# Kernel optimization log

Hardware: AMD Instinct MI355X
Metric: run time of the kernel (lower is better)

## Reference

```python
import jax, jax.numpy as jnp
import numpy as np

SIZE = 4096
DOWN = SIZE // 16  # reduction_factor = 16 -> 256
N_TASKS = 16
BATCH = 2048
INIT_STD = 0.01


def setup_inputs() -> dict:
    key = jax.random.key(0)
    k_x, k_t, k_wd, k_wu = jax.random.split(key, 4)
    x = jax.random.normal(k_x, (BATCH, SIZE), dtype=jnp.float32)
    task_id = jax.random.randint(k_t, (BATCH,), 0, N_TASKS)
    # Stacked per-task adapter params (init: normal(std=0.01) weights, zero bias)
    Wd = jax.random.normal(k_wd, (N_TASKS, SIZE, DOWN), dtype=jnp.float32) * INIT_STD
    bd = jnp.zeros((N_TASKS, DOWN), dtype=jnp.float32)
    Wu = jax.random.normal(k_wu, (N_TASKS, DOWN, SIZE), dtype=jnp.float32) * INIT_STD
    bu = jnp.zeros((N_TASKS, SIZE), dtype=jnp.float32)
    return {"x": x, "task_id": task_id, "Wd": Wd, "bd": bd, "Wu": Wu, "bu": bu}


def reference(x, task_id, Wd, bd, Wu, bu):
    # Down-projection for all tasks, then select each sample's routed task.
    # [B, T, DOWN] is small (B*T*256), cheaper than gathering [B, SIZE, DOWN] weights.
    down_all = jnp.einsum('bd,tdh->bth', x, Wd) + bd[None]
    down = jnp.take_along_axis(down_all, task_id[:, None, None], axis=1)[:, 0]  # [B, DOWN]
    act = jax.nn.silu(down)
    # Up-projection for all tasks, select routed task. [B, T, SIZE]
    up_all = jnp.einsum('bh,thd->btd', act, Wu) + bu[None]
    up = jnp.take_along_axis(up_all, task_id[:, None, None], axis=1)[:, 0]  # [B, SIZE]
    return x + up  # residual=True (default)
```

## Files before the change

### kernel.cpp

```cpp
#include <hip/hip_runtime.h>

#define BATCH 2048
#define SIZE 4096
#define DOWN 256
#define NTASK 16
#define KC 16
#define KCHUNK (SIZE / KC)

typedef _Float16 half8 __attribute__((ext_vector_type(8)));
typedef _Float16 half4 __attribute__((ext_vector_type(4)));
typedef float floatx4 __attribute__((ext_vector_type(4)));

__device__ __forceinline__ int imin(int a, int b) { return a < b ? a : b; }

__global__ __launch_bounds__(256) void sort_kernel(const int* __restrict__ task_id,
                                                   int* __restrict__ taskOff,
                                                   int* __restrict__ sortedIdx,
                                                   int* __restrict__ taskOfPos) {
    __shared__ int cnt[NTASK];
    __shared__ int base[NTASK + 1];
    __shared__ int cur[NTASK];
    int tid = threadIdx.x;
    if (tid < NTASK) cnt[tid] = 0;
    __syncthreads();
    for (int i = tid; i < BATCH; i += 256) atomicAdd(&cnt[task_id[i]], 1);
    __syncthreads();
    if (tid == 0) {
        int s = 0;
        for (int t = 0; t < NTASK; t++) { base[t] = s; s += cnt[t]; }
        base[NTASK] = s;
    }
    __syncthreads();
    if (tid < NTASK) { cur[tid] = base[tid]; taskOff[tid] = base[tid]; }
    if (tid == 0) taskOff[NTASK] = BATCH;
    __syncthreads();
    for (int i = tid; i < BATCH; i += 256) {
        int t = task_id[i];
        int p = atomicAdd(&cur[t], 1);
        sortedIdx[p] = i;
        taskOfPos[p] = t;
    }
}

__global__ __launch_bounds__(256, 2) void gemm1_kernel(const float* __restrict__ x,
                                                       const float* __restrict__ Wd,
                                                       const int* __restrict__ taskOff,
                                                       const int* __restrict__ sortedIdx,
                                                       _Float16* __restrict__ partial) {
    int task = blockIdx.x >> 1, z = blockIdx.x & 1, kc = blockIdx.y;
    int rowStart = taskOff[task];
    int nrows = taskOff[task + 1] - rowStart;
    if (nrows <= 0) return;

    __shared__ half8 A_lds[32][64];
    __shared__ half8 B_lds[4][64][8];

    int tid = threadIdx.x;
    int wave = tid >> 6, lane = tid & 63, quad = lane >> 4, l15 = lane & 15;
    int kbase = kc * KCHUNK;
    const float* Wdt = Wd + (size_t)task * SIZE * DOWN;
    int arow = tid >> 2, ac = tid & 3;

    for (int r0 = z * 64; r0 < nrows; r0 += 128) {
        __syncthreads();
        {
            int asrc = sortedIdx[rowStart + imin(r0 + arow, nrows - 1)];
            const float* xr = x + (size_t)asrc * SIZE + kbase;
            floatx4 f[16];
#pragma unroll
            for (int i = 0; i < 16; i++)
                f[i] = *(const floatx4*)(xr + i * 16 + ac * 4);
#pragma unroll
            for (int i = 0; i < 16; i++) {
                half4 h;
                h[0] = (_Float16)f[i][0]; h[1] = (_Float16)f[i][1];
                h[2] = (_Float16)f[i][2]; h[3] = (_Float16)f[i][3];
                int kg = i * 2 + (ac >> 1);
                *((half4*)(&A_lds[kg][arow]) + (ac & 1)) = h;
            }
        }
        __syncthreads();

        floatx4 acc[4][4];
#pragma unroll
        for (int mi = 0; mi < 4; mi++)
#pragma unroll
            for (int ni = 0; ni < 4; ni++) acc[mi][ni] = (floatx4){0.f, 0.f, 0.f, 0.f};

        for (int kb = 0; kb < KCHUNK; kb += 64) {
            floatx4 fb[16];
            const float* bs =
                Wdt + (size_t)(kbase + kb + quad * 16) * DOWN + wave * 64 + l15 * 4;
#pragma unroll
            for (int j = 0; j < 16; j++) fb[j] = *(const floatx4*)(bs + (size_t)j * DOWN);
#pragma unroll
            for (int g = 0; g < 2; g++)
#pragma unroll
                for (int n2 = 0; n2 < 4; n2++) {
                    half8 h;
#pragma unroll
                    for (int e = 0; e < 8; e++) h[e] = (_Float16)fb[g * 8 + e][n2];
                    B_lds[wave][l15 * 4 + n2][quad * 2 + g] = h;
                }
#pragma unroll
            for (int ks = 0; ks < 2; ks++) {
                int kg = (kb >> 3) + ks * 4 + quad;
                half8 a[4], b[4];
#pragma unroll
                for (int i = 0; i < 4; i++) a[i] = A_lds[kg][i * 16 + l15];
#pragma unroll
                for (int i = 0; i < 4; i++) b[i] = B_lds[wave][i * 16 + l15][ks * 4 + quad];
#pragma unroll
                for (int mi = 0; mi < 4; mi++)
#pragma unroll
                    for (int ni = 0; ni < 4; ni++)
                        acc[mi][ni] = __builtin_amdgcn_mfma_f32_16x16x32_f16(
                            a[mi], b[ni], acc[mi][ni], 0, 0, 0);
            }
        }
#pragma unroll
        for (int mi = 0; mi < 4; mi++) {
#pragma unroll
            for (int reg = 0; reg < 4; reg++) {
                int r = r0 + mi * 16 + quad * 4 + reg;
                if (r < nrows) {
                    size_t rowoff = ((size_t)kc * BATCH + (rowStart + r)) * DOWN;
#pragma unroll
                    for (int ni = 0; ni < 4; ni++) {
                        int h = wave * 64 + ni * 16 + l15;
                        partial[rowoff + h] = (_Float16)acc[mi][ni][reg];
                    }
                }
            }
        }
    }
}

__global__ __launch_bounds__(256) void silu_kernel(const _Float16* __restrict__ partial,
                                                   const float* __restrict__ bd,
                                                   const int* __restrict__ taskOfPos,
                                                   _Float16* __restrict__ act) {
    int idx = blockIdx.x * 256 + threadIdx.x;
    int s = idx >> 5;
    int h = (idx & 31) * 8;
    int t = taskOfPos[s];
    floatx4 b0 = *(const floatx4*)(bd + t * DOWN + h);
    floatx4 b1 = *(const floatx4*)(bd + t * DOWN + h + 4);
    float v[8];
    v[0] = b0[0]; v[1] = b0[1]; v[2] = b0[2]; v[3] = b0[3];
    v[4] = b1[0]; v[5] = b1[1]; v[6] = b1[2]; v[7] = b1[3];
#pragma unroll
    for (int kc = 0; kc < KC; kc++) {
        half8 p = *(const half8*)(partial + ((size_t)kc * BATCH + s) * DOWN + h);
#pragma unroll
        for (int j = 0; j < 8; j++) v[j] += (float)p[j];
    }
    half8 o;
#pragma unroll
    for (int j = 0; j < 8; j++) {
        float sv = v[j] / (1.0f + __expf(-v[j]));
        o[j] = (_Float16)sv;
    }
    *(half8*)(act + (size_t)s * DOWN + h) = o;
}

__global__ __launch_bounds__(256, 2) void gemm2_kernel(const _Float16* __restrict__ act,
                                                       const float* __restrict__ Wu,
                                                       const float* __restrict__ bu,
                                                       const float* __restrict__ x,
                                                       const int* __restrict__ taskOff,
                                                       const int* __restrict__ sortedIdx,
                                                       float* __restrict__ out) {
    int nt = blockIdx.x >> 1, z = blockIdx.x & 1, task = blockIdx.y;
    int rowStart = taskOff[task];
    int nrows = taskOff[task + 1] - rowStart;
    if (nrows <= 0) return;

    __shared__ half8 A_lds[32][64];
    __shared__ half8 B_lds[4][64][8];

    int tid = threadIdx.x;
    int wave = tid >> 6, lane = tid & 63, quad = lane >> 4, l15 = lane & 15;
    int ncol0 = nt * 256;
    const float* Wut = Wu + (size_t)task * DOWN * SIZE;
    int arow = tid >> 2, ac = tid & 3;

    for (int r0 = z * 64; r0 < nrows; r0 += 128) {
        __syncthreads();
        {
            int s_a = rowStart + imin(r0 + arow, nrows - 1);
            const _Float16* ar = act + (size_t)s_a * DOWN;
#pragma unroll
            for (int j = 0; j < 8; j++) {
                int kg = j * 4 + ac;
                A_lds[kg][arow] = *(const half8*)(ar + kg * 8);
            }
        }
        __syncthreads();

        floatx4 acc[4][4];
#pragma unroll
        for (int mi = 0; mi < 4; mi++)
#pragma unroll
            for (int ni = 0; ni < 4; ni++) acc[mi][ni] = (floatx4){0.f, 0.f, 0.f, 0.f};

        for (int kb = 0; kb < DOWN; kb += 64) {
            floatx4 fb[16];
            const float* bs =
                Wut + (size_t)(kb + quad * 16) * SIZE + ncol0 + wave * 64 + l15 * 4;
#pragma unroll
            for (int j = 0; j < 16; j++) fb[j] = *(const floatx4*)(bs + (size_t)j * SIZE);
#pragma unroll
            for (int g = 0; g < 2; g++)
#pragma unroll
                for (int n2 = 0; n2 < 4; n2++) {
                    half8 h;
#pragma unroll
                    for (int e = 0; e < 8; e++) h[e] = (_Float16)fb[g * 8 + e][n2];
                    B_lds[wave][l15 * 4 + n2][quad * 2 + g] = h;
                }
#pragma unroll
            for (int ks = 0; ks < 2; ks++) {
                int kg = (kb >> 3) + ks * 4 + quad;
                half8 a[4], b[4];
#pragma unroll
                for (int i = 0; i < 4; i++) a[i] = A_lds[kg][i * 16 + l15];
#pragma unroll
                for (int i = 0; i < 4; i++) b[i] = B_lds[wave][i * 16 + l15][ks * 4 + quad];
#pragma unroll
                for (int mi = 0; mi < 4; mi++)
#pragma unroll
                    for (int ni = 0; ni < 4; ni++)
                        acc[mi][ni] = __builtin_amdgcn_mfma_f32_16x16x32_f16(
                            a[mi], b[ni], acc[mi][ni], 0, 0, 0);
            }
        }
#pragma unroll
        for (int mi = 0; mi < 4; mi++) {
#pragma unroll
            for (int reg = 0; reg < 4; reg++) {
                int r = r0 + mi * 16 + quad * 4 + reg;
                if (r < nrows) {
                    int b = sortedIdx[rowStart + r];
                    const float* xr = x + (size_t)b * SIZE;
                    float* outr = out + (size_t)b * SIZE;
#pragma unroll
                    for (int ni = 0; ni < 4; ni++) {
                        int n = ncol0 + wave * 64 + ni * 16 + l15;
                        outr[n] = acc[mi][ni][reg] + bu[task * SIZE + n] + xr[n];
                    }
                }
            }
        }
    }
}

extern "C" void kernel_launch(void* const* d_in, const int* in_sizes, int n_in,
                              void* d_out, int out_size, void* d_ws, size_t ws_size,
                              hipStream_t stream) {
    const float* x       = (const float*)d_in[0];
    const int*   task_id = (const int*)d_in[1];
    const float* Wd      = (const float*)d_in[2];
    const float* bd      = (const float*)d_in[3];
    const float* Wu      = (const float*)d_in[4];
    const float* bu      = (const float*)d_in[5];
    float* out = (float*)d_out;

    _Float16* partial = (_Float16*)d_out;
    _Float16* act     = (_Float16*)d_ws;
    int* taskOff   = (int*)(act + (size_t)BATCH * DOWN);
    int* sortedIdx = taskOff + 32;
    int* taskOfPos = sortedIdx + BATCH;

    sort_kernel<<<1, 256, 0, stream>>>(task_id, taskOff, sortedIdx, taskOfPos);
    gemm1_kernel<<<dim3(NTASK * 2, KC), 256, 0, stream>>>(x, Wd, taskOff, sortedIdx, partial);
    silu_kernel<<<(BATCH * DOWN / 8) / 256, 256, 0, stream>>>(partial, bd, taskOfPos, act);
    gemm2_kernel<<<dim3(32, NTASK), 256, 0, stream>>>(act, Wu, bu, x, taskOff,
                                                      sortedIdx, out);
}
```

Measured before the change: 254.5 us.

## Pipeline both GEMMs with async global-to-LDS loads and triple buffering

Both GEMM kernels now stage fp32 A and B tiles straight into LDS with global_load_lds in a 3-stage ring over BK=16 k-slices. Explicit vmcnt waits and barriers let loads for later stages overlap with the MFMAs. The fp32-to-fp16 conversion moves to the LDS read side, and the MFMA shape changes to 16x16x16. The activation buffer is now fp32 so gemm2 can async-load it directly, which doubles its traffic, and LDS reads of strided B columns may cause bank conflicts and extra conversion work.

New measurement: 255.3 us. No clear change (+0.3%).

```diff
diff --git a/kernel.cpp b/kernel.cpp
--- a/kernel.cpp
+++ b/kernel.cpp
@@ -6,12 +6,27 @@
 #define NTASK 16
 #define KC 16
 #define KCHUNK (SIZE / KC)
-
-typedef _Float16 half8 __attribute__((ext_vector_type(8)));
+#define BK 16
+
 typedef _Float16 half4 __attribute__((ext_vector_type(4)));
 typedef float floatx4 __attribute__((ext_vector_type(4)));
 
 __device__ __forceinline__ int imin(int a, int b) { return a < b ? a : b; }
+
+__device__ __forceinline__ void async16(void* lds, const void* g) {
+    __builtin_amdgcn_global_load_lds((const __attribute__((address_space(1))) unsigned int*)g,
+                                     (__attribute__((address_space(3))) unsigned int*)lds,
+                                     16, 0, 0);
+}
+
+#define WAITV5() asm volatile("s_waitcnt vmcnt(5)" ::: "memory")
+#define WAITV0() asm volatile("s_waitcnt vmcnt(0)" ::: "memory")
+#define SBAR()                             \
+    do {                                   \
+        __builtin_amdgcn_sched_barrier(0); \
+        __builtin_amdgcn_s_barrier();      \
+        __builtin_amdgcn_sched_barrier(0); \
+    } while (0)
 
 __global__ __launch_bounds__(256) void sort_kernel(const int* __restrict__ task_id,
                                                    int* __restrict__ taskOff,
@@ -52,72 +67,70 @@
     int nrows = taskOff[task + 1] - rowStart;
     if (nrows <= 0) return;
 
-    __shared__ half8 A_lds[32][64];
-    __shared__ half8 B_lds[4][64][8];
+    __shared__ float Bf[3][BK][DOWN];
+    __shared__ float Af[3][4][64][4];
 
     int tid = threadIdx.x;
     int wave = tid >> 6, lane = tid & 63, quad = lane >> 4, l15 = lane & 15;
     int kbase = kc * KCHUNK;
-    const float* Wdt = Wd + (size_t)task * SIZE * DOWN;
-    int arow = tid >> 2, ac = tid & 3;
+    const float* Wdt = Wd + (size_t)task * SIZE * DOWN + (size_t)kbase * DOWN;
 
     for (int r0 = z * 64; r0 < nrows; r0 += 128) {
-        __syncthreads();
-        {
-            int asrc = sortedIdx[rowStart + imin(r0 + arow, nrows - 1)];
-            const float* xr = x + (size_t)asrc * SIZE + kbase;
-            floatx4 f[16];
-#pragma unroll
-            for (int i = 0; i < 16; i++)
-                f[i] = *(const floatx4*)(xr + i * 16 + ac * 4);
-#pragma unroll
-            for (int i = 0; i < 16; i++) {
+        int sidx = sortedIdx[rowStart + imin(r0 + lane, nrows - 1)];
+        const float* aptr = x + (size_t)sidx * SIZE + kbase;
+        const float* bptr = Wdt + (size_t)(wave * 4) * DOWN + lane * 4;
+
+#define G1_ISSUE(T, BI)                                                  \
+        {                                                                \
+            const float* bs_ = bptr + (size_t)(T) * BK * DOWN;           \
+            async16(&Bf[BI][wave * 4 + 0][0], bs_);                      \
+            async16(&Bf[BI][wave * 4 + 1][0], bs_ + DOWN);               \
+            async16(&Bf[BI][wave * 4 + 2][0], bs_ + 2 * DOWN);           \
+            async16(&Bf[BI][wave * 4 + 3][0], bs_ + 3 * DOWN);           \
+            async16(&Af[BI][wave][0][0], aptr + (T) * BK + wave * 4);    \
+        }
+
+        floatx4 acc[4][4];
+#pragma unroll
+        for (int mi = 0; mi < 4; mi++)
+#pragma unroll
+            for (int ni = 0; ni < 4; ni++) acc[mi][ni] = (floatx4){0.f, 0.f, 0.f, 0.f};
+
+        G1_ISSUE(0, 0);
+        G1_ISSUE(1, 1);
+        int buf = 0, nb = 2;
+        for (int t = 0; t < 16; t++) {
+            if (t < 15) { WAITV5(); } else { WAITV0(); }
+            SBAR();
+            if (t < 14) { G1_ISSUE(t + 2, nb); }
+            half4 a[4], b[4];
+#pragma unroll
+            for (int mi = 0; mi < 4; mi++) {
+                floatx4 v = *(const floatx4*)&Af[buf][quad][mi * 16 + l15][0];
                 half4 h;
-                h[0] = (_Float16)f[i][0]; h[1] = (_Float16)f[i][1];
-                h[2] = (_Float16)f[i][2]; h[3] = (_Float16)f[i][3];
-                int kg = i * 2 + (ac >> 1);
-                *((half4*)(&A_lds[kg][arow]) + (ac & 1)) = h;
-            }
-        }
-        __syncthreads();
-
-        floatx4 acc[4][4];
-#pragma unroll
-        for (int mi = 0; mi < 4; mi++)
-#pragma unroll
-            for (int ni = 0; ni < 4; ni++) acc[mi][ni] = (floatx4){0.f, 0.f, 0.f, 0.f};
-
-        for (int kb = 0; kb < KCHUNK; kb += 64) {
-            floatx4 fb[16];
-            const float* bs =
-                Wdt + (size_t)(kbase + kb + quad * 16) * DOWN + wave * 64 + l15 * 4;
-#pragma unroll
-            for (int j = 0; j < 16; j++) fb[j] = *(const floatx4*)(bs + (size_t)j * DOWN);
-#pragma unroll
-            for (int g = 0; g < 2; g++)
-#pragma unroll
-                for (int n2 = 0; n2 < 4; n2++) {
-                    half8 h;
-#pragma unroll
-                    for (int e = 0; e < 8; e++) h[e] = (_Float16)fb[g * 8 + e][n2];
-                    B_lds[wave][l15 * 4 + n2][quad * 2 + g] = h;
-                }
-#pragma unroll
-            for (int ks = 0; ks < 2; ks++) {
-                int kg = (kb >> 3) + ks * 4 + quad;
-                half8 a[4], b[4];
-#pragma unroll
-                for (int i = 0; i < 4; i++) a[i] = A_lds[kg][i * 16 + l15];
-#pragma unroll
-                for (int i = 0; i < 4; i++) b[i] = B_lds[wave][i * 16 + l15][ks * 4 + quad];
-#pragma unroll
-                for (int mi = 0; mi < 4; mi++)
-#pragma unroll
-                    for (int ni = 0; ni < 4; ni++)
-                        acc[mi][ni] = __builtin_amdgcn_mfma_f32_16x16x32_f16(
-                            a[mi], b[ni], acc[mi][ni], 0, 0, 0);
-            }
-        }
+                h[0] = (_Float16)v[0]; h[1] = (_Float16)v[1];
+                h[2] = (_Float16)v[2]; h[3] = (_Float16)v[3];
+                a[mi] = h;
+            }
+#pragma unroll
+            for (int ni = 0; ni < 4; ni++) {
+                int n = wave * 64 + ni * 16 + l15;
+                half4 h;
+#pragma unroll
+                for (int e = 0; e < 4; e++) h[e] = (_Float16)Bf[buf][quad * 4 + e][n];
+                b[ni] = h;
+            }
+#pragma unroll
+            for (int mi = 0; mi < 4; mi++)
+#pragma unroll
+                for (int ni = 0; ni < 4; ni++)
+                    acc[mi][ni] = __builtin_amdgcn_mfma_f32_16x16x16f16(
+                        a[mi], b[ni], acc[mi][ni], 0, 0, 0);
+            buf = (buf == 2) ? 0 : buf + 1;
+            nb = (nb == 2) ? 0 : nb + 1;
+        }
+        SBAR();
+#undef G1_ISSUE
 #pragma unroll
         for (int mi = 0; mi < 4; mi++) {
 #pragma unroll
@@ -139,7 +152,8 @@
 __global__ __launch_bounds__(256) void silu_kernel(const _Float16* __restrict__ partial,
                                                    const float* __restrict__ bd,
                                                    const int* __restrict__ taskOfPos,
-                                                   _Float16* __restrict__ act) {
+                                                   float* __restrict__ act) {
+    typedef _Float16 half8 __attribute__((ext_vector_type(8)));
     int idx = blockIdx.x * 256 + threadIdx.x;
     int s = idx >> 5;
     int h = (idx & 31) * 8;
@@ -155,16 +169,16 @@
 #pragma unroll
         for (int j = 0; j < 8; j++) v[j] += (float)p[j];
     }
-    half8 o;
-#pragma unroll
-    for (int j = 0; j < 8; j++) {
-        float sv = v[j] / (1.0f + __expf(-v[j]));
-        o[j] = (_Float16)sv;
-    }
-    *(half8*)(act + (size_t)s * DOWN + h) = o;
-}
-
-__global__ __launch_bounds__(256, 2) void gemm2_kernel(const _Float16* __restrict__ act,
+    floatx4 o0, o1;
+#pragma unroll
+    for (int j = 0; j < 4; j++) o0[j] = v[j] / (1.0f + __expf(-v[j]));
+#pragma unroll
+    for (int j = 0; j < 4; j++) o1[j] = v[j + 4] / (1.0f + __expf(-v[j + 4]));
+    *(floatx4*)(act + (size_t)s * DOWN + h) = o0;
+    *(floatx4*)(act + (size_t)s * DOWN + h + 4) = o1;
+}
+
+__global__ __launch_bounds__(256, 2) void gemm2_kernel(const float* __restrict__ act,
                                                        const float* __restrict__ Wu,
                                                        const float* __restrict__ bu,
                                                        const float* __restrict__ x,
@@ -176,27 +190,27 @@
     int nrows = taskOff[task + 1] - rowStart;
     if (nrows <= 0) return;
 
-    __shared__ half8 A_lds[32][64];
-    __shared__ half8 B_lds[4][64][8];
+    __shared__ float Bf[3][BK][256];
+    __shared__ float Af[3][4][64][4];
 
     int tid = threadIdx.x;
     int wave = tid >> 6, lane = tid & 63, quad = lane >> 4, l15 = lane & 15;
     int ncol0 = nt * 256;
-    const float* Wut = Wu + (size_t)task * DOWN * SIZE;
-    int arow = tid >> 2, ac = tid & 3;
+    const float* Wut = Wu + (size_t)task * DOWN * SIZE + ncol0;
 
     for (int r0 = z * 64; r0 < nrows; r0 += 128) {
-        __syncthreads();
-        {
-            int s_a = rowStart + imin(r0 + arow, nrows - 1);
-            const _Float16* ar = act + (size_t)s_a * DOWN;
-#pragma unroll
-            for (int j = 0; j < 8; j++) {
-                int kg = j * 4 + ac;
-                A_lds[kg][arow] = *(const half8*)(ar + kg * 8);
-            }
-        }
-        __syncthreads();
+        const float* aptr = act + (size_t)(rowStart + imin(r0 + lane, nrows - 1)) * DOWN;
+        const float* bptr = Wut + (size_t)(wave * 4) * SIZE + lane * 4;
+
+#define G2_ISSUE(T, BI)                                                  \
+        {                                                                \
+            const float* bs_ = bptr + (size_t)(T) * BK * SIZE;           \
+            async16(&Bf[BI][wave * 4 + 0][0], bs_);                      \
+            async16(&Bf[BI][wave * 4 + 1][0], bs_ + SIZE);               \
+            async16(&Bf[BI][wave * 4 + 2][0], bs_ + 2 * SIZE);           \
+            async16(&Bf[BI][wave * 4 + 3][0], bs_ + 3 * SIZE);           \
+            async16(&Af[BI][wave][0][0], aptr + (T) * BK + wave * 4);    \
+        }
 
         floatx4 acc[4][4];
 #pragma unroll
@@ -204,37 +218,41 @@
 #pragma unroll
             for (int ni = 0; ni < 4; ni++) acc[mi][ni] = (floatx4){0.f, 0.f, 0.f, 0.f};
 
-        for (int kb = 0; kb < DOWN; kb += 64) {
-            floatx4 fb[16];
-            const float* bs =
-                Wut + (size_t)(kb + quad * 16) * SIZE + ncol0 + wave * 64 + l15 * 4;
-#pragma unroll
-            for (int j = 0; j < 16; j++) fb[j] = *(const floatx4*)(bs + (size_t)j * SIZE);
-#pragma unroll
-            for (int g = 0; g < 2; g++)
-#pragma unroll
-                for (int n2 = 0; n2 < 4; n2++) {
-                    half8 h;
-#pragma unroll
-                    for (int e = 0; e < 8; e++) h[e] = (_Float16)fb[g * 8 + e][n2];
-                    B_lds[wave][l15 * 4 + n2][quad * 2 + g] = h;
-                }
-#pragma unroll
-            for (int ks = 0; ks < 2; ks++) {
-                int kg = (kb >> 3) + ks * 4 + quad;
-                half8 a[4], b[4];
-#pragma unroll
-                for (int i = 0; i < 4; i++) a[i] = A_lds[kg][i * 16 + l15];
-#pragma unroll
-                for (int i = 0; i < 4; i++) b[i] = B_lds[wave][i * 16 + l15][ks * 4 + quad];
-#pragma unroll
-                for (int mi = 0; mi < 4; mi++)
-#pragma unroll
-                    for (int ni = 0; ni < 4; ni++)
-                        acc[mi][ni] = __builtin_amdgcn_mfma_f32_16x16x32_f16(
-                            a[mi], b[ni], acc[mi][ni], 0, 0, 0);
-            }
-        }
+        G2_ISSUE(0, 0);
+        G2_ISSUE(1, 1);
+        int buf = 0, nb = 2;
+        for (int t = 0; t < 16; t++) {
+            if (t < 15) { WAITV5(); } else { WAITV0(); }
+            SBAR();
+            if (t < 14) { G2_ISSUE(t + 2, nb); }
+            half4 a[4], b[4];
+#pragma unroll
+            for (int mi = 0; mi < 4; mi++) {
+                floatx4 v = *(const floatx4*)&Af[buf][quad][mi * 16 + l15][0];
+                half4 h;
+                h[0] = (_Float16)v[0]; h[1] = (_Float16)v[1];
+                h[2] = (_Float16)v[2]; h[3] = (_Float16)v[3];
+                a[mi] = h;
+            }
+#pragma unroll
+            for (int ni = 0; ni < 4; ni++) {
+                int n = wave * 64 + ni * 16 + l15;
+                half4 h;
+#pragma unroll
+                for (int e = 0; e < 4; e++) h[e] = (_Float16)Bf[buf][quad * 4 + e][n];
+                b[ni] = h;
+            }
+#pragma unroll
+            for (int mi = 0; mi < 4; mi++)
+#pragma unroll
+                for (int ni = 0; ni < 4; ni++)
+                    acc[mi][ni] = __builtin_amdgcn_mfma_f32_16x16x16f16(
+                        a[mi], b[ni], acc[mi][ni], 0, 0, 0);
+            buf = (buf == 2) ? 0 : buf + 1;
+            nb = (nb == 2) ? 0 : nb + 1;
+        }
+        SBAR();
+#undef G2_ISSUE
 #pragma unroll
         for (int mi = 0; mi < 4; mi++) {
 #pragma unroll
@@ -267,14 +285,16 @@
     float* out = (float*)d_out;
 
     _Float16* partial = (_Float16*)d_out;
-    _Float16* act     = (_Float16*)d_ws;
+    float* act        = (float*)d_ws;
     int* taskOff   = (int*)(act + (size_t)BATCH * DOWN);
     int* sortedIdx = taskOff + 32;
     int* taskOfPos = sortedIdx + BATCH;
 
     sort_kernel<<<1, 256, 0, stream>>>(task_id, taskOff, sortedIdx, taskOfPos);
-    gemm1_kernel<<<dim3(NTASK * 2, KC), 256, 0, stream>>>(x, Wd, taskOff, sortedIdx, partial);
-    silu_kernel<<<(BATCH * DOWN / 8) / 256, 256, 0, stream>>>(partial, bd, taskOfPos, act);
+    gemm1_kernel<<<dim3(NTASK * 2, KC), 256, 0, stream>>>(x, Wd, taskOff, sortedIdx,
+                                                          partial);
+    silu_kernel<<<(BATCH * DOWN / 8) / 256, 256, 0, stream>>>(partial, bd, taskOfPos,
+                                                              act);
     gemm2_kernel<<<dim3(32, NTASK), 256, 0, stream>>>(act, Wu, bu, x, taskOff,
                                                       sortedIdx, out);
 }
```
